# Kernel optimization log

Hardware: AMD Instinct MI355X
Metric: run time of the kernel (lower is better)

Reference implementation:

```python
import jax, jax.numpy as jnp
import numpy as np

N_KV_HEADS = 8
MAX_CONTEXT = 8192
HEAD_DIM = 128  # dim // n_heads = 4096 // 32
N_NEW = 16


def setup_inputs() -> dict:
    key = jax.random.key(0)
    k1, k2, k3, k4, k5 = jax.random.split(key, 5)
    pos_ids = jnp.sort(jax.random.randint(k1, (N_NEW,), 0, MAX_CONTEXT, dtype=jnp.int64))
    k = jax.random.normal(k2, (1, N_KV_HEADS, N_NEW, HEAD_DIM), dtype=jnp.float32)
    v = jax.random.normal(k3, (1, N_KV_HEADS, N_NEW, HEAD_DIM), dtype=jnp.float32)
    k_cache = jax.random.normal(k4, (1, N_KV_HEADS, MAX_CONTEXT, HEAD_DIM), dtype=jnp.float32)
    v_cache = jax.random.normal(k5, (1, N_KV_HEADS, MAX_CONTEXT, HEAD_DIM), dtype=jnp.float32)
    return {"pos_ids": pos_ids, "k": k, "v": v, "k_cache": k_cache, "v_cache": v_cache}


def reference(pos_ids, k, v, k_cache, v_cache):
    # Functional equivalent of: clone cache, then cache[:, :, pos_ids, :] = new.
    # jnp .at[].set on the seq axis produces a fresh (copied) buffer, matching
    # the torch clone-then-scatter semantics.
    kout = k_cache.at[:, :, pos_ids, :].set(k)
    vout = v_cache.at[:, :, pos_ids, :].set(v)
    return (kout, vout)
```

## Files before the change

kernel.cpp:

```cpp
#include <hip/hip_runtime.h>


#define NNEW 16

__global__ __launch_bounds__(256) void kv_update_kernel(
    const int* __restrict__ pos,
    const float4* __restrict__ knew,
    const float4* __restrict__ vnew,
    const float4* __restrict__ kcache,
    const float4* __restrict__ vcache,
    float4* __restrict__ out)
{
    const unsigned int i = blockIdx.x * 256u + threadIdx.x;

    const unsigned int is_v = i >> 21;
    const unsigned int j = i & ((1u << 21) - 1u);
    const unsigned int h  = j >> 18;
    const int          s  = (int)((j >> 5) & 8191u);
    const unsigned int d4 = j & 31u;

    int match = -1;
#pragma unroll
    for (int n = 0; n < NNEW; ++n) {
        if (pos[n] == s) match = n;
    }

    float4 val;
    if (match >= 0) {
        const float4* __restrict__ src = is_v ? vnew : knew;
        val = src[(h * NNEW + (unsigned)match) * 32u + d4];
    } else {
        const float4* __restrict__ src = is_v ? vcache : kcache;
        val = src[j];
    }
    out[i] = val;
}

extern "C" void kernel_launch(void* const* d_in, const int* in_sizes, int n_in,
                              void* d_out, int out_size, void* d_ws, size_t ws_size,
                              hipStream_t stream) {
    const int*    pos    = (const int*)   d_in[0];
    const float4* knew   = (const float4*)d_in[1];
    const float4* vnew   = (const float4*)d_in[2];
    const float4* kcache = (const float4*)d_in[3];
    const float4* vcache = (const float4*)d_in[4];
    float4*       out    = (float4*)d_out;

    const unsigned int nblocks = (1u << 22) / 256u;
    kv_update_kernel<<<nblocks, 256, 0, stream>>>(pos, knew, vnew, kcache, vcache, out);
}
```

Before: 119.1 us.

## Copy caches with hipMemcpyAsync then scatter new rows in small kernel

Replaces the fused copy-or-select kernel with two device-to-device memcpys of the K and V caches followed by a small scatter kernel that writes only the 16 new rows per head. When positions repeat, only the last one is written, matching scatter semantics. The aim is to drop the per-element 16-way position comparison and let the runtime copy engine or blit kernel handle the bulk copy. The cost is two extra launches and a serial dependency, and the memcpy path may be slower than a tuned copy kernel.

```diff
diff --git a/kernel.cpp b/kernel.cpp
--- a/kernel.cpp
+++ b/kernel.cpp
@@ -2,38 +2,37 @@
 
 
 #define NNEW 16
+#define NH   8
+#define CTX  8192
+#define HD4  32
 
-__global__ __launch_bounds__(256) void kv_update_kernel(
+__global__ __launch_bounds__(256) void kv_scatter_kernel(
     const int* __restrict__ pos,
     const float4* __restrict__ knew,
     const float4* __restrict__ vnew,
-    const float4* __restrict__ kcache,
-    const float4* __restrict__ vcache,
     float4* __restrict__ out)
 {
-    const unsigned int i = blockIdx.x * 256u + threadIdx.x;
+    const unsigned i = blockIdx.x * 256u + threadIdx.x;
+    const unsigned is_v = i >> 12;
+    const unsigned j    = i & 4095u;
+    const unsigned h    = j >> 9;
+    const int      n    = (int)((j >> 5) & 15u);
+    const unsigned d4   = j & 31u;
 
-    const unsigned int is_v = i >> 21;
-    const unsigned int j = i & ((1u << 21) - 1u);
-    const unsigned int h  = j >> 18;
-    const int          s  = (int)((j >> 5) & 8191u);
-    const unsigned int d4 = j & 31u;
+    const int s = pos[n];
+    bool shadowed = false;
+#pragma unroll
+    for (int m = 0; m < NNEW; ++m) {
+        shadowed |= (m > n) & (pos[m] == s);
+    }
+    if (shadowed) return;
 
-    int match = -1;
-#pragma unroll
-    for (int n = 0; n < NNEW; ++n) {
-        if (pos[n] == s) match = n;
-    }
+    const float4* __restrict__ src = is_v ? vnew : knew;
+    const float4 val = src[j];
 
-    float4 val;
-    if (match >= 0) {
-        const float4* __restrict__ src = is_v ? vnew : knew;
-        val = src[(h * NNEW + (unsigned)match) * 32u + d4];
-    } else {
-        const float4* __restrict__ src = is_v ? vcache : kcache;
-        val = src[j];
-    }
-    out[i] = val;
+    const unsigned dst = is_v * (NH * CTX * HD4)
+                       + (h * CTX + (unsigned)s) * HD4 + d4;
+    out[dst] = val;
 }
 
 extern "C" void kernel_launch(void* const* d_in, const int* in_sizes, int n_in,
@@ -42,10 +41,15 @@
     const int*    pos    = (const int*)   d_in[0];
     const float4* knew   = (const float4*)d_in[1];
     const float4* vnew   = (const float4*)d_in[2];
-    const float4* kcache = (const float4*)d_in[3];
-    const float4* vcache = (const float4*)d_in[4];
-    float4*       out    = (float4*)d_out;
+    const void*   kcache = d_in[3];
+    const void*   vcache = d_in[4];
 
-    const unsigned int nblocks = (1u << 22) / 256u;
-    kv_update_kernel<<<nblocks, 256, 0, stream>>>(pos, knew, vnew, kcache, vcache, out);
+    const size_t cache_bytes = (size_t)NH * CTX * 128 * sizeof(float);
+
+    hipMemcpyAsync(d_out, kcache, cache_bytes, hipMemcpyDeviceToDevice, stream);
+    hipMemcpyAsync((char*)d_out + cache_bytes, vcache, cache_bytes,
+                   hipMemcpyDeviceToDevice, stream);
+
+    kv_scatter_kernel<<<8192 / 256, 256, 0, stream>>>(
+        pos, knew, vnew, (float4*)d_out);
 }
```

Result: slower. 128.0 us (+7.5%).
